# Kernel optimization log

Hardware: AMD Instinct MI355X
Metric: run time of the kernel (lower is better)

The kernel has to match this reference:

```python
import jax, jax.numpy as jnp
import numpy as np

B, T, D, K = 16, 4096, 512, 128
ALPHA_MIN = 1e-06
OMEGA_MAX = float(np.pi)
SN_EPS = 1e-06


def setup_inputs() -> dict:
    key = jax.random.key(0)
    ks = jax.random.split(key, 7)
    x = jax.random.normal(ks[0], (B, T, D), jnp.float32)
    # irregular positive step sizes, mean ~ 1/T like the uniform-grid default
    dt = jax.random.uniform(ks[1], (B, T), jnp.float32, minval=0.1, maxval=1.9) * (1.0 / T)
    # replicate reset_parameters: target_alpha ~ U(0.01, 0.2), raw = log(expm1(alpha - alpha_min))
    target_alpha = jax.random.uniform(ks[2], (K,), jnp.float32, minval=0.01, maxval=0.2)
    s_real_raw = jnp.log(jnp.expm1(jnp.maximum(target_alpha - ALPHA_MIN, 1e-08)))
    s_imag = jax.random.uniform(ks[3], (K,), jnp.float32, minval=-np.pi, maxval=np.pi)
    # kaiming-uniform-ish proj weight [K, D] and bias [K]
    W = jax.random.normal(ks[4], (K, D), jnp.float32) * (1.0 / np.sqrt(D))
    bound = 1.0 / np.sqrt(D)
    bias = jax.random.uniform(ks[5], (K,), jnp.float32, minval=-bound, maxval=bound)
    b_log = jnp.zeros((K,), jnp.float32)  # torch stores [1,1,K]; broadcasting is identical
    u_sn = jax.random.normal(ks[6], (K,), jnp.float32)  # spectral-norm power-iteration vector
    return {"x": x, "dt": dt, "s_real_raw": s_real_raw, "s_imag": s_imag,
            "W": W, "bias": bias, "b_log": b_log, "u_sn": u_sn}


def _spectral_normalize(W, u):
    # one power iteration, u/v detached (as torch.nn.utils.spectral_norm does)
    v = W.T @ u
    v = v / (jnp.linalg.norm(v) + SN_EPS)
    u2 = W @ v
    u2 = u2 / (jnp.linalg.norm(u2) + SN_EPS)
    u2 = jax.lax.stop_gradient(u2)
    v = jax.lax.stop_gradient(v)
    sigma = u2 @ (W @ v)
    return W / sigma


def reference(x, dt, s_real_raw, s_imag, W, bias, b_log, u_sn):
    # x: [B,T,D], dt: [B,T] -> lap_feats [B,T,2K]
    alpha = jax.nn.softplus(s_real_raw) + ALPHA_MIN          # [K] strictly positive decay
    omega = jnp.clip(s_imag, -OMEGA_MAX, OMEGA_MAX)          # [K]
    Wsn = _spectral_normalize(W, u_sn)
    u = jnp.einsum('btd,kd->btk', x, Wsn) + bias             # spectral-norm projection
    dt3 = dt[..., None]                                      # [B,T,1]
    rho = jnp.exp(-alpha * dt3)                              # [B,T,K]
    theta = omega * dt3
    cos_t, sin_t = jnp.cos(theta), jnp.sin(theta)
    b_gain = jnp.exp(b_log)                                  # [K]
    inj = (1.0 - rho) * (b_gain * u)                         # [B,T,K]

    def step(carry, inp):
        c, s = carry
        r, ct, st, it = inp
        c_new = r * (c * ct - s * st) + it
        s_new = r * (c * st + s * ct) + it
        return (c_new, s_new), (c_new, s_new)

    seq = (jnp.moveaxis(rho, 1, 0), jnp.moveaxis(cos_t, 1, 0),
           jnp.moveaxis(sin_t, 1, 0), jnp.moveaxis(inj, 1, 0))  # each [T,B,K]
    init = (jnp.zeros((x.shape[0], K), x.dtype), jnp.zeros((x.shape[0], K), x.dtype))
    _, (C, S) = jax.lax.scan(step, init, seq)
    C = jnp.moveaxis(C, 0, 1)  # [B,T,K]
    S = jnp.moveaxis(S, 0, 1)
    return jnp.concatenate([C, S], axis=-1)
```

## Files before the change

kernel.cpp:

```cpp
#include <hip/hip_runtime.h>
#include <stdint.h>

#define BB 16
#define TT 4096
#define DDIM 512
#define KK 128
#define TCB 128
#define NCB (TT / TCB)
#define PI_F 3.14159265358979323846f

typedef unsigned short u16;
typedef __attribute__((ext_vector_type(8))) short short8;
typedef __attribute__((ext_vector_type(4))) float f32x4;

__device__ __forceinline__ uint32_t cvt_bf16_rn(float f) {
  uint32_t u = __float_as_uint(f);
  return (u + 0x7FFFu + ((u >> 16) & 1u)) >> 16;
}
__device__ __forceinline__ uint32_t pack2(float a, float b) {
  return cvt_bf16_rn(a) | (cvt_bf16_rn(b) << 16);
}
__device__ __forceinline__ uint4 pack8(const float4 f0, const float4 f1) {
  uint4 r;
  r.x = pack2(f0.x, f0.y);
  r.y = pack2(f0.z, f0.w);
  r.z = pack2(f1.x, f1.y);
  r.w = pack2(f1.z, f1.w);
  return r;
}
__device__ __forceinline__ float bf16_to_f32(u16 v) {
  return __uint_as_float(((uint32_t)v) << 16);
}
__device__ __forceinline__ void gload_lds16(const void* g, void* l) {
  __builtin_amdgcn_global_load_lds(
      (const __attribute__((address_space(1))) void*)g,
      (__attribute__((address_space(3))) void*)l, 16, 0, 0);
}

__global__ __launch_bounds__(256) void k_prep(
    const float* __restrict__ W, const float* __restrict__ u_sn,
    const float* __restrict__ s_real_raw, const float* __restrict__ s_imag,
    const float* __restrict__ bias, const float* __restrict__ b_log,
    const float* __restrict__ dt,
    float* __restrict__ params, u16* __restrict__ Wp, float* __restrict__ ct) {
  int gb = blockIdx.x;
  int tid = threadIdx.x;
  if (gb < 64) {
    int idx = gb * 256 + tid;
    int k = idx >> 7;
    int d = (idx & 127) * 4;
    float4 v = *(const float4*)&W[(size_t)k * DDIM + d];
    int tile = d >> 6, dl = d & 63;
    int slot = (dl >> 3) ^ (k & 7);
    int e = dl & 7;
    size_t base = (size_t)tile * 8192 + k * 64 + slot * 8 + e;
    uint2 p;
    p.x = pack2(v.x, v.y);
    p.y = pack2(v.z, v.w);
    *(uint2*)&Wp[base] = p;
  } else if (gb < 80) {
    __shared__ float sc[256];
    int b = gb - 64;
    const float* row = dt + (size_t)b * TT;
    float* orow = ct + (size_t)b * TT;
    float loc[16];
    float s = 0.f;
    int base = tid * 16;
    for (int i = 0; i < 16; ++i) { s += row[base + i]; loc[i] = s; }
    sc[tid] = s;
    __syncthreads();
    for (int off = 1; off < 256; off <<= 1) {
      float v = (tid >= off) ? sc[tid - off] : 0.f;
      __syncthreads();
      sc[tid] += v;
      __syncthreads();
    }
    float excl = sc[tid] - s;
    for (int i = 0; i < 16; ++i) orow[base + i] = excl + loc[i];
  } else {
    __shared__ float su[KK];
    __shared__ float sv[DDIM];
    __shared__ float red[4];
    __shared__ float s_sig;
    if (tid < KK) su[tid] = u_sn[tid];
    __syncthreads();
    for (int rep = 0; rep < 2; ++rep) {
      int d = tid + rep * 256;
      float acc = 0.f;
      for (int k = 0; k < KK; ++k) acc += W[k * DDIM + d] * su[k];
      sv[d] = acc;
    }
    __syncthreads();
    float nn = 0.f;
    for (int rep = 0; rep < 2; ++rep) { float v = sv[tid + rep * 256]; nn += v * v; }
    for (int off = 32; off > 0; off >>= 1) nn += __shfl_down(nn, off, 64);
    if ((tid & 63) == 0) red[tid >> 6] = nn;
    __syncthreads();
    float vn2 = red[0] + red[1] + red[2] + red[3];
    __syncthreads();
    float vinv = 1.f / (sqrtf(vn2) + 1e-6f);
    for (int rep = 0; rep < 2; ++rep) sv[tid + rep * 256] *= vinv;
    __syncthreads();
    float wv = 0.f;
    if (tid < KK) {
      const float* wrow = W + (size_t)tid * DDIM;
      for (int d = 0; d < DDIM; ++d) wv += wrow[d] * sv[d];
    }
    float q = wv * wv;
    for (int off = 32; off > 0; off >>= 1) q += __shfl_down(q, off, 64);
    if ((tid & 63) == 0) red[tid >> 6] = q;
    __syncthreads();
    if (tid == 0) {
      float wn2 = red[0] + red[1] + red[2] + red[3];
      s_sig = wn2 / (sqrtf(wn2) + 1e-6f);
    }
    __syncthreads();
    if (tid < KK) {
      float inv_sigma = 1.f / s_sig;
      float sr = s_real_raw[tid];
      float alpha = ((sr > 20.f) ? sr : log1pf(expf(sr))) + 1e-6f;
      float om = fminf(fmaxf(s_imag[tid], -PI_F), PI_F);
      float bg = expf(b_log[tid]);
      params[tid] = alpha;
      params[KK + tid] = om;
      params[2 * KK + tid] = bg * inv_sigma;
      params[3 * KK + tid] = bg * bias[tid];
    }
  }
}

__global__ __launch_bounds__(512, 4) void k_gemm(
    const float* __restrict__ x, const u16* __restrict__ Wp,
    const float* __restrict__ dt, const float* __restrict__ ct,
    const float* __restrict__ params, u16* __restrict__ itvb,
    float* __restrict__ csum_re, float* __restrict__ csum_im) {
  __shared__ __align__(16) u16 smem[32768];

  const int chunk = blockIdx.x, b = blockIdx.y;
  const int tid = threadIdx.x;
  const int wv = tid >> 6, l = tid & 63;
  const int lm = l & 15, lg = l >> 4;
  const int kw = wv & 1, tw = wv >> 1;
  const int t0 = chunk * TCB;

  const int xr = tid >> 2, xq = (tid & 3) * 16;
  const size_t xbase = ((size_t)b * TT + t0 + xr) * DDIM + xq;
  const int xs0 = ((xq >> 3) ^ (xr & 7)) * 8;
  const int xs1 = (((xq >> 3) + 1) ^ (xr & 7)) * 8;

  f32x4 acc[2][4];
#pragma unroll
  for (int m = 0; m < 2; ++m)
#pragma unroll
    for (int n = 0; n < 4; ++n) acc[m][n] = (f32x4)(0.0f);

  {
    const char* wsg = (const char*)Wp + (size_t)tid * 16;
    char* wd = (char*)smem + 32768 + tid * 16;
    gload_lds16(wsg, wd);
    gload_lds16(wsg + 8192, wd + 8192);
    const float* xp = x + xbase;
    float4 f0 = *(const float4*)(xp + 0);
    float4 f1 = *(const float4*)(xp + 4);
    float4 f2 = *(const float4*)(xp + 8);
    float4 f3 = *(const float4*)(xp + 12);
    *(uint4*)&smem[xr * 64 + xs0] = pack8(f0, f1);
    *(uint4*)&smem[xr * 64 + xs1] = pack8(f2, f3);
  }
  __syncthreads();

  int cur = 0;
  for (int it = 0; it < 8; ++it) {
    float4 f0, f1, f2, f3;
    if (it < 7) {
      const float* xp = x + xbase + (it + 1) * 64;
      f0 = *(const float4*)(xp + 0);
      f1 = *(const float4*)(xp + 4);
      f2 = *(const float4*)(xp + 8);
      f3 = *(const float4*)(xp + 12);
      const char* wsg = (const char*)Wp + (size_t)(it + 1) * 16384 + tid * 16;
      char* wd = (char*)smem + 32768 + (cur ^ 1) * 16384 + tid * 16;
      gload_lds16(wsg, wd);
      gload_lds16(wsg + 8192, wd + 8192);
    }
    __builtin_amdgcn_sched_barrier(0);
    {
      const u16* xb = smem + cur * 8192;
      const u16* wb = smem + 16384 + cur * 8192;
#pragma unroll
      for (int ks = 0; ks < 2; ++ks) {
        short8 fa[2], fb[4];
#pragma unroll
        for (int m = 0; m < 2; ++m) {
          int row = tw * 32 + m * 16 + lm;
          int sw = ((ks * 4 + lg) ^ (row & 7)) * 8;
          fa[m] = *(const short8*)&xb[row * 64 + sw];
        }
#pragma unroll
        for (int n = 0; n < 4; ++n) {
          int row = kw * 64 + n * 16 + lm;
          int sw = ((ks * 4 + lg) ^ (row & 7)) * 8;
          fb[n] = *(const short8*)&wb[row * 64 + sw];
        }
#pragma unroll
        for (int m = 0; m < 2; ++m)
#pragma unroll
          for (int n = 0; n < 4; ++n)
            acc[m][n] = __builtin_amdgcn_mfma_f32_16x16x32_bf16(fa[m], fb[n], acc[m][n], 0, 0, 0);
      }
    }
    __builtin_amdgcn_sched_barrier(0);
    if (it < 7) {
      u16* xb = smem + (cur ^ 1) * 8192;
      *(uint4*)&xb[xr * 64 + xs0] = pack8(f0, f1);
      *(uint4*)&xb[xr * 64 + xs1] = pack8(f2, f3);
    }
    __syncthreads();
    cur ^= 1;
  }

  float* totr = (float*)smem;
  float* toti = (float*)smem + 512;
  u16* litv = smem + 8192;

  float dtv[2][4], ctv[2][4];
#pragma unroll
  for (int m = 0; m < 2; ++m)
#pragma unroll
    for (int r = 0; r < 4; ++r) {
      int t = t0 + tw * 32 + m * 16 + lg * 4 + r;
      dtv[m][r] = dt[(size_t)b * TT + t];
      ctv[m][r] = ct[(size_t)b * TT + t];
    }

#pragma unroll
  for (int n = 0; n < 4; ++n) {
    int k = kw * 64 + n * 16 + lm;
    float pal = params[k], pom = params[KK + k];
    float pc1 = params[2 * KK + k], pc2 = params[3 * KK + k];
    float sr = 0.f, si2 = 0.f;
#pragma unroll
    for (int m = 0; m < 2; ++m)
#pragma unroll
      for (int r = 0; r < 4; ++r) {
        float g = acc[m][n][r];
        float a = pal * dtv[m][r];
        float omr = a * (1.f - a * (0.5f - a * (1.f / 6.f)));
        float itv = omr * (pc1 * g + pc2);
        int tl = tw * 32 + m * 16 + lg * 4 + r;
        litv[tl * KK + k] = (u16)cvt_bf16_rn(itv);
        float e = __expf(pal * ctv[m][r]);
        float sn, cs;
        __sincosf(pom * ctv[m][r], &sn, &cs);
        sr += itv * e * cs;
        si2 -= itv * e * sn;
      }
    sr += __shfl_xor(sr, 16, 64);
    sr += __shfl_xor(sr, 32, 64);
    si2 += __shfl_xor(si2, 16, 64);
    si2 += __shfl_xor(si2, 32, 64);
    if (lg == 0) { totr[tw * KK + k] = sr; toti[tw * KK + k] = si2; }
  }
  __syncthreads();

  if (tid < 256) {
    int v = tid & 127;
    float* src = (tid < 128) ? totr : toti;
    float* dst = (tid < 128) ? csum_re : csum_im;
    dst[((size_t)b * NCB + chunk) * KK + v] =
        (src[v] + src[KK + v]) + (src[2 * KK + v] + src[3 * KK + v]);
  }
  {
    int row = tid >> 4;
    int c8 = (tid & 15) * 8;
#pragma unroll
    for (int rr = 0; rr < 4; ++rr) {
      int tr = rr * 32 + row;
      uint4 v = *(const uint4*)&litv[tr * KK + c8];
      *(uint4*)&itvb[((size_t)b * TT + t0 + tr) * KK + c8] = v;
    }
  }
}

__global__ __launch_bounds__(512) void k_final(
    const u16* __restrict__ itvb, const float* __restrict__ ct,
    const float* __restrict__ params,
    const float* __restrict__ csum_re, const float* __restrict__ csum_im,
    float* __restrict__ out) {
  __shared__ float prer[KK], prei[KK];
  __shared__ float segr[4][KK], segi[4][KK];
  const int chunk = blockIdx.x, b = blockIdx.y;
  const int tid = threadIdx.x;
  const int k = tid & 127, tseg = tid >> 7;
  const int tbase = chunk * TCB + tseg * 32;

  if (tid < 256) {
    int v = tid & 127;
    const float* srcp = (tid < 128) ? csum_re : csum_im;
    float* dstp = (tid < 128) ? prer : prei;
    size_t base = (size_t)b * NCB * KK + v;
    float a0 = 0.f, a1 = 0.f, a2 = 0.f, a3 = 0.f;
    int c = 0;
    for (; c + 4 <= chunk; c += 4) {
      a0 += srcp[base + (size_t)(c + 0) * KK];
      a1 += srcp[base + (size_t)(c + 1) * KK];
      a2 += srcp[base + (size_t)(c + 2) * KK];
      a3 += srcp[base + (size_t)(c + 3) * KK];
    }
    for (; c < chunk; ++c) a0 += srcp[base + (size_t)c * KK];
    dstp[v] = (a0 + a1) + (a2 + a3);
  }

  const float pal = params[k], pom = params[KK + k];
  float sr = 0.f, si = 0.f;
#pragma unroll 4
  for (int i = 0; i < 32; ++i) {
    int t = tbase + i;
    float itv = bf16_to_f32(itvb[((size_t)b * TT + t) * KK + k]);
    float ctv = ct[(size_t)b * TT + t];
    float e = __expf(pal * ctv);
    float sn, cs;
    __sincosf(pom * ctv, &sn, &cs);
    sr += itv * e * cs;
    si -= itv * e * sn;
  }
  segr[tseg][k] = sr;
  segi[tseg][k] = si;
  __syncthreads();
  float cr = prer[k], ci = prei[k];
  for (int s = 0; s < tseg; ++s) { cr += segr[s][k]; ci += segi[s][k]; }
#pragma unroll 4
  for (int i = 0; i < 32; ++i) {
    int t = tbase + i;
    float itv = bf16_to_f32(itvb[((size_t)b * TT + t) * KK + k]);
    float ctv = ct[(size_t)b * TT + t];
    float e = __expf(pal * ctv);
    float sn, cs;
    __sincosf(pom * ctv, &sn, &cs);
    cr += itv * e * cs;
    ci -= itv * e * sn;
    float dec = __builtin_amdgcn_rcpf(e);
    float Rw = dec * (cs * cr - sn * ci);
    float Iw = dec * (cs * ci + sn * cr);
    size_t rowb = ((size_t)b * TT + t) * (2 * KK);
    out[rowb + k] = Rw - Iw;
    out[rowb + KK + k] = Rw + Iw;
  }
}

extern "C" void kernel_launch(void* const* d_in, const int* in_sizes, int n_in,
                              void* d_out, int out_size, void* d_ws, size_t ws_size,
                              hipStream_t stream) {
  const float* x    = (const float*)d_in[0];
  const float* dt   = (const float*)d_in[1];
  const float* srr  = (const float*)d_in[2];
  const float* si   = (const float*)d_in[3];
  const float* W    = (const float*)d_in[4];
  const float* bias = (const float*)d_in[5];
  const float* blog = (const float*)d_in[6];
  const float* usn  = (const float*)d_in[7];
  float* out = (float*)d_out;
  float* ws = (float*)d_ws;

  float* params  = ws;
  float* ct      = ws + 4 * KK;
  float* csum_re = ct + (size_t)BB * TT;
  float* csum_im = csum_re + (size_t)BB * NCB * KK;
  u16*   Wp      = (u16*)(csum_im + (size_t)BB * NCB * KK);
  u16*   itvb    = Wp + 65536;

  k_prep<<<81, 256, 0, stream>>>(W, usn, srr, si, bias, blog, dt, params, Wp, ct);
  k_gemm<<<dim3(NCB, BB), 512, 0, stream>>>(x, Wp, dt, ct, params, itvb,
                                            csum_re, csum_im);
  k_final<<<dim3(NCB, BB), 512, 0, stream>>>(itvb, ct, params,
                                             csum_re, csum_im, out);
}
```

Before: 69.58 us.

## Deepen GEMM x-prefetch pipeline and vectorize final scan over four channels per thread

The projection kernel now prefetches x two K-steps ahead into alternating register sets. Its full __syncthreads is replaced by explicit vmcnt/lgkmcnt waits plus s_barrier, so global loads stay in flight across the MFMA phase. The final kernel gives each thread four adjacent channels and an 8-step time segment (16 segments instead of 4). It uses 8-byte bf16 loads and float4 output stores in place of scalar accesses. This cuts per-element memory instructions and shortens the serial per-thread loop, at the cost of more register pressure and a longer serial prefix sum over segments.

```diff
diff --git a/kernel.cpp b/kernel.cpp
--- a/kernel.cpp
+++ b/kernel.cpp
@@ -27,9 +27,6 @@
   r.z = pack2(f1.x, f1.y);
   r.w = pack2(f1.z, f1.w);
   return r;
-}
-__device__ __forceinline__ float bf16_to_f32(u16 v) {
-  return __uint_as_float(((uint32_t)v) << 16);
 }
 __device__ __forceinline__ void gload_lds16(const void* g, void* l) {
   __builtin_amdgcn_global_load_lds(
@@ -154,39 +151,63 @@
 #pragma unroll
     for (int n = 0; n < 4; ++n) acc[m][n] = (f32x4)(0.0f);
 
+  float4 xa[4], xb[4];
+  const char* wsrc = (const char*)Wp + (size_t)tid * 16;
+  char* wd0 = (char*)smem + 32768 + tid * 16;
+  char* wd1 = wd0 + 16384;
+
   {
-    const char* wsg = (const char*)Wp + (size_t)tid * 16;
-    char* wd = (char*)smem + 32768 + tid * 16;
-    gload_lds16(wsg, wd);
-    gload_lds16(wsg + 8192, wd + 8192);
+    gload_lds16(wsrc, wd0);
+    gload_lds16(wsrc + 8192, wd0 + 8192);
     const float* xp = x + xbase;
-    float4 f0 = *(const float4*)(xp + 0);
-    float4 f1 = *(const float4*)(xp + 4);
-    float4 f2 = *(const float4*)(xp + 8);
-    float4 f3 = *(const float4*)(xp + 12);
-    *(uint4*)&smem[xr * 64 + xs0] = pack8(f0, f1);
-    *(uint4*)&smem[xr * 64 + xs1] = pack8(f2, f3);
-  }
-  __syncthreads();
-
-  int cur = 0;
-  for (int it = 0; it < 8; ++it) {
-    float4 f0, f1, f2, f3;
-    if (it < 7) {
-      const float* xp = x + xbase + (it + 1) * 64;
-      f0 = *(const float4*)(xp + 0);
-      f1 = *(const float4*)(xp + 4);
-      f2 = *(const float4*)(xp + 8);
-      f3 = *(const float4*)(xp + 12);
-      const char* wsg = (const char*)Wp + (size_t)(it + 1) * 16384 + tid * 16;
-      char* wd = (char*)smem + 32768 + (cur ^ 1) * 16384 + tid * 16;
+    xa[0] = *(const float4*)(xp + 0);
+    xa[1] = *(const float4*)(xp + 4);
+    xa[2] = *(const float4*)(xp + 8);
+    xa[3] = *(const float4*)(xp + 12);
+    gload_lds16(wsrc + 16384, wd1);
+    gload_lds16(wsrc + 16384 + 8192, wd1 + 8192);
+    const float* xp1 = x + xbase + 64;
+    xb[0] = *(const float4*)(xp1 + 0);
+    xb[1] = *(const float4*)(xp1 + 4);
+    xb[2] = *(const float4*)(xp1 + 8);
+    xb[3] = *(const float4*)(xp1 + 12);
+    __builtin_amdgcn_sched_barrier(0);
+    asm volatile("s_waitcnt vmcnt(6)" ::: "memory");
+    __builtin_amdgcn_sched_barrier(0);
+    *(uint4*)&smem[xr * 64 + xs0] = pack8(xa[0], xa[1]);
+    *(uint4*)&smem[xr * 64 + xs1] = pack8(xa[2], xa[3]);
+    asm volatile("s_waitcnt lgkmcnt(0)" ::: "memory");
+    __builtin_amdgcn_s_barrier();
+    __builtin_amdgcn_sched_barrier(0);
+  }
+
+#pragma unroll
+  for (int j = 0; j < 8; ++j) {
+    const int p = j & 1;
+    if (j >= 1 && j <= 6) {
+      const char* wsg = (const char*)Wp + (size_t)(j + 1) * 16384 + tid * 16;
+      char* wd = (char*)smem + 32768 + ((j + 1) & 1) * 16384 + tid * 16;
       gload_lds16(wsg, wd);
       gload_lds16(wsg + 8192, wd + 8192);
     }
+    if (j <= 5) {
+      const float* xp = x + xbase + (size_t)(j + 2) * 64;
+      if (p == 0) {
+        xa[0] = *(const float4*)(xp + 0);
+        xa[1] = *(const float4*)(xp + 4);
+        xa[2] = *(const float4*)(xp + 8);
+        xa[3] = *(const float4*)(xp + 12);
+      } else {
+        xb[0] = *(const float4*)(xp + 0);
+        xb[1] = *(const float4*)(xp + 4);
+        xb[2] = *(const float4*)(xp + 8);
+        xb[3] = *(const float4*)(xp + 12);
+      }
+    }
     __builtin_amdgcn_sched_barrier(0);
     {
-      const u16* xb = smem + cur * 8192;
-      const u16* wb = smem + 16384 + cur * 8192;
+      const u16* xbuf = smem + p * 8192;
+      const u16* wbuf = smem + 16384 + p * 8192;
 #pragma unroll
       for (int ks = 0; ks < 2; ++ks) {
         short8 fa[2], fb[4];
@@ -194,13 +215,13 @@
         for (int m = 0; m < 2; ++m) {
           int row = tw * 32 + m * 16 + lm;
           int sw = ((ks * 4 + lg) ^ (row & 7)) * 8;
-          fa[m] = *(const short8*)&xb[row * 64 + sw];
+          fa[m] = *(const short8*)&xbuf[row * 64 + sw];
         }
 #pragma unroll
         for (int n = 0; n < 4; ++n) {
           int row = kw * 64 + n * 16 + lm;
           int sw = ((ks * 4 + lg) ^ (row & 7)) * 8;
-          fb[n] = *(const short8*)&wb[row * 64 + sw];
+          fb[n] = *(const short8*)&wbuf[row * 64 + sw];
         }
 #pragma unroll
         for (int m = 0; m < 2; ++m)
@@ -210,14 +231,24 @@
       }
     }
     __builtin_amdgcn_sched_barrier(0);
-    if (it < 7) {
-      u16* xb = smem + (cur ^ 1) * 8192;
-      *(uint4*)&xb[xr * 64 + xs0] = pack8(f0, f1);
-      *(uint4*)&xb[xr * 64 + xs1] = pack8(f2, f3);
-    }
-    __syncthreads();
-    cur ^= 1;
-  }
+    if (j <= 6) {
+      if (j == 6) asm volatile("s_waitcnt vmcnt(0)" ::: "memory");
+      else        asm volatile("s_waitcnt vmcnt(4)" ::: "memory");
+      __builtin_amdgcn_sched_barrier(0);
+      u16* xw = smem + (p ^ 1) * 8192;
+      if (((j + 1) & 1) == 0) {
+        *(uint4*)&xw[xr * 64 + xs0] = pack8(xa[0], xa[1]);
+        *(uint4*)&xw[xr * 64 + xs1] = pack8(xa[2], xa[3]);
+      } else {
+        *(uint4*)&xw[xr * 64 + xs0] = pack8(xb[0], xb[1]);
+        *(uint4*)&xw[xr * 64 + xs1] = pack8(xb[2], xb[3]);
+      }
+      asm volatile("s_waitcnt lgkmcnt(0)" ::: "memory");
+      __builtin_amdgcn_s_barrier();
+      __builtin_amdgcn_sched_barrier(0);
+    }
+  }
+  __syncthreads();
 
   float* totr = (float*)smem;
   float* toti = (float*)smem + 512;
@@ -288,11 +319,11 @@
     const float* __restrict__ csum_re, const float* __restrict__ csum_im,
     float* __restrict__ out) {
   __shared__ float prer[KK], prei[KK];
-  __shared__ float segr[4][KK], segi[4][KK];
+  __shared__ float segr[16][KK], segi[16][KK];
   const int chunk = blockIdx.x, b = blockIdx.y;
   const int tid = threadIdx.x;
-  const int k = tid & 127, tseg = tid >> 7;
-  const int tbase = chunk * TCB + tseg * 32;
+  const int k4 = (tid & 31) * 4, tseg = tid >> 5;
+  const int tbase = chunk * TCB + tseg * 8;
 
   if (tid < 256) {
     int v = tid & 127;
@@ -311,40 +342,68 @@
     dstp[v] = (a0 + a1) + (a2 + a3);
   }
 
-  const float pal = params[k], pom = params[KK + k];
-  float sr = 0.f, si = 0.f;
-#pragma unroll 4
-  for (int i = 0; i < 32; ++i) {
+  float4 pal4 = *(const float4*)&params[k4];
+  float4 pom4 = *(const float4*)&params[KK + k4];
+  float pal[4] = {pal4.x, pal4.y, pal4.z, pal4.w};
+  float pom[4] = {pom4.x, pom4.y, pom4.z, pom4.w};
+
+  float sr[4] = {0.f, 0.f, 0.f, 0.f}, si[4] = {0.f, 0.f, 0.f, 0.f};
+#pragma unroll
+  for (int i = 0; i < 8; ++i) {
     int t = tbase + i;
-    float itv = bf16_to_f32(itvb[((size_t)b * TT + t) * KK + k]);
     float ctv = ct[(size_t)b * TT + t];
-    float e = __expf(pal * ctv);
-    float sn, cs;
-    __sincosf(pom * ctv, &sn, &cs);
-    sr += itv * e * cs;
-    si -= itv * e * sn;
-  }
-  segr[tseg][k] = sr;
-  segi[tseg][k] = si;
+    uint2 iv = *(const uint2*)&itvb[((size_t)b * TT + t) * KK + k4];
+    float it[4] = {__uint_as_float(iv.x << 16), __uint_as_float(iv.x & 0xFFFF0000u),
+                   __uint_as_float(iv.y << 16), __uint_as_float(iv.y & 0xFFFF0000u)};
+#pragma unroll
+    for (int c = 0; c < 4; ++c) {
+      float e = __expf(pal[c] * ctv);
+      float sn, cs;
+      __sincosf(pom[c] * ctv, &sn, &cs);
+      sr[c] += it[c] * e * cs;
+      si[c] -= it[c] * e * sn;
+    }
+  }
+  *(float4*)&segr[tseg][k4] = make_float4(sr[0], sr[1], sr[2], sr[3]);
+  *(float4*)&segi[tseg][k4] = make_float4(si[0], si[1], si[2], si[3]);
   __syncthreads();
-  float cr = prer[k], ci = prei[k];
-  for (int s = 0; s < tseg; ++s) { cr += segr[s][k]; ci += segi[s][k]; }
-#pragma unroll 4
-  for (int i = 0; i < 32; ++i) {
+  float cr[4], ci[4];
+  {
+    float4 p0 = *(const float4*)&prer[k4];
+    float4 p1 = *(const float4*)&prei[k4];
+    cr[0] = p0.x; cr[1] = p0.y; cr[2] = p0.z; cr[3] = p0.w;
+    ci[0] = p1.x; ci[1] = p1.y; ci[2] = p1.z; ci[3] = p1.w;
+  }
+  for (int s = 0; s < tseg; ++s) {
+    float4 a = *(const float4*)&segr[s][k4];
+    float4 bb = *(const float4*)&segi[s][k4];
+    cr[0] += a.x; cr[1] += a.y; cr[2] += a.z; cr[3] += a.w;
+    ci[0] += bb.x; ci[1] += bb.y; ci[2] += bb.z; ci[3] += bb.w;
+  }
+#pragma unroll
+  for (int i = 0; i < 8; ++i) {
     int t = tbase + i;
-    float itv = bf16_to_f32(itvb[((size_t)b * TT + t) * KK + k]);
     float ctv = ct[(size_t)b * TT + t];
-    float e = __expf(pal * ctv);
-    float sn, cs;
-    __sincosf(pom * ctv, &sn, &cs);
-    cr += itv * e * cs;
-    ci -= itv * e * sn;
-    float dec = __builtin_amdgcn_rcpf(e);
-    float Rw = dec * (cs * cr - sn * ci);
-    float Iw = dec * (cs * ci + sn * cr);
+    uint2 iv = *(const uint2*)&itvb[((size_t)b * TT + t) * KK + k4];
+    float it[4] = {__uint_as_float(iv.x << 16), __uint_as_float(iv.x & 0xFFFF0000u),
+                   __uint_as_float(iv.y << 16), __uint_as_float(iv.y & 0xFFFF0000u)};
+    float C4[4], S4[4];
+#pragma unroll
+    for (int c = 0; c < 4; ++c) {
+      float e = __expf(pal[c] * ctv);
+      float sn, cs;
+      __sincosf(pom[c] * ctv, &sn, &cs);
+      cr[c] += it[c] * e * cs;
+      ci[c] -= it[c] * e * sn;
+      float dec = __builtin_amdgcn_rcpf(e);
+      float Rw = dec * (cs * cr[c] - sn * ci[c]);
+      float Iw = dec * (cs * ci[c] + sn * cr[c]);
+      C4[c] = Rw - Iw;
+      S4[c] = Rw + Iw;
+    }
     size_t rowb = ((size_t)b * TT + t) * (2 * KK);
-    out[rowb + k] = Rw - Iw;
-    out[rowb + KK + k] = Rw + Iw;
+    *(float4*)&out[rowb + k4] = make_float4(C4[0], C4[1], C4[2], C4[3]);
+    *(float4*)&out[rowb + KK + k4] = make_float4(S4[0], S4[1], S4[2], S4[3]);
   }
 }
 
```

Result: slower. 71.18 us (+2.3%).

## Vectorize final scan pass over 4 channels and cache twiddles in registers

Applied to the files above, without the earlier changes.

The final kernel now gives each thread 4 adjacent channels over 8 timesteps instead of 1 channel over 32, with 16 segments per chunk. Loads of the bf16 input and stores of the output become vectorized. The exp/sincos factors and the input values are kept in registers from the first pass, so the second pass does not recompute transcendentals or reload data, and it gets the decay inverse from the squared magnitude of the cached factor. The prep kernel also splits the W·v matvec across all 256 threads, which adds register pressure and a longer serial prefix over 16 segments.

```diff
diff --git a/kernel.cpp b/kernel.cpp
--- a/kernel.cpp
+++ b/kernel.cpp
@@ -27,9 +27,6 @@
   r.z = pack2(f1.x, f1.y);
   r.w = pack2(f1.z, f1.w);
   return r;
-}
-__device__ __forceinline__ float bf16_to_f32(u16 v) {
-  return __uint_as_float(((uint32_t)v) << 16);
 }
 __device__ __forceinline__ void gload_lds16(const void* g, void* l) {
   __builtin_amdgcn_global_load_lds(
@@ -81,6 +78,7 @@
     __shared__ float su[KK];
     __shared__ float sv[DDIM];
     __shared__ float red[4];
+    __shared__ float wred[256];
     __shared__ float s_sig;
     if (tid < KK) su[tid] = u_sn[tid];
     __syncthreads();
@@ -101,11 +99,16 @@
     float vinv = 1.f / (sqrtf(vn2) + 1e-6f);
     for (int rep = 0; rep < 2; ++rep) sv[tid + rep * 256] *= vinv;
     __syncthreads();
+    {
+      int k = tid & 127, q = tid >> 7;
+      const float* wrow = W + (size_t)k * DDIM + q * 256;
+      float p = 0.f;
+      for (int d = 0; d < 256; ++d) p += wrow[d] * sv[q * 256 + d];
+      wred[tid] = p;
+    }
+    __syncthreads();
     float wv = 0.f;
-    if (tid < KK) {
-      const float* wrow = W + (size_t)tid * DDIM;
-      for (int d = 0; d < DDIM; ++d) wv += wrow[d] * sv[d];
-    }
+    if (tid < KK) wv = wred[tid] + wred[tid + 128];
     float q = wv * wv;
     for (int off = 32; off > 0; off >>= 1) q += __shfl_down(q, off, 64);
     if ((tid & 63) == 0) red[tid >> 6] = q;
@@ -288,11 +291,11 @@
     const float* __restrict__ csum_re, const float* __restrict__ csum_im,
     float* __restrict__ out) {
   __shared__ float prer[KK], prei[KK];
-  __shared__ float segr[4][KK], segi[4][KK];
+  __shared__ float segr[16][KK], segi[16][KK];
   const int chunk = blockIdx.x, b = blockIdx.y;
   const int tid = threadIdx.x;
-  const int k = tid & 127, tseg = tid >> 7;
-  const int tbase = chunk * TCB + tseg * 32;
+  const int k4 = (tid & 31) * 4, tseg = tid >> 5;
+  const int tbase = chunk * TCB + tseg * 8;
 
   if (tid < 256) {
     int v = tid & 127;
@@ -311,40 +314,68 @@
     dstp[v] = (a0 + a1) + (a2 + a3);
   }
 
-  const float pal = params[k], pom = params[KK + k];
-  float sr = 0.f, si = 0.f;
-#pragma unroll 4
-  for (int i = 0; i < 32; ++i) {
+  float4 pal4 = *(const float4*)&params[k4];
+  float4 pom4 = *(const float4*)&params[KK + k4];
+  float pal[4] = {pal4.x, pal4.y, pal4.z, pal4.w};
+  float pom[4] = {pom4.x, pom4.y, pom4.z, pom4.w};
+
+  uint2 iv8[8];
+  float fr[8][4], fi[8][4];
+  float sr[4] = {0.f, 0.f, 0.f, 0.f}, si[4] = {0.f, 0.f, 0.f, 0.f};
+#pragma unroll
+  for (int i = 0; i < 8; ++i) {
     int t = tbase + i;
-    float itv = bf16_to_f32(itvb[((size_t)b * TT + t) * KK + k]);
     float ctv = ct[(size_t)b * TT + t];
-    float e = __expf(pal * ctv);
-    float sn, cs;
-    __sincosf(pom * ctv, &sn, &cs);
-    sr += itv * e * cs;
-    si -= itv * e * sn;
-  }
-  segr[tseg][k] = sr;
-  segi[tseg][k] = si;
+    iv8[i] = *(const uint2*)&itvb[((size_t)b * TT + t) * KK + k4];
+    float it[4] = {__uint_as_float(iv8[i].x << 16), __uint_as_float(iv8[i].x & 0xFFFF0000u),
+                   __uint_as_float(iv8[i].y << 16), __uint_as_float(iv8[i].y & 0xFFFF0000u)};
+#pragma unroll
+    for (int c = 0; c < 4; ++c) {
+      float e = __expf(pal[c] * ctv);
+      float sn, cs;
+      __sincosf(pom[c] * ctv, &sn, &cs);
+      fr[i][c] = e * cs;
+      fi[i][c] = e * sn;
+      sr[c] += it[c] * fr[i][c];
+      si[c] -= it[c] * fi[i][c];
+    }
+  }
+  *(float4*)&segr[tseg][k4] = make_float4(sr[0], sr[1], sr[2], sr[3]);
+  *(float4*)&segi[tseg][k4] = make_float4(si[0], si[1], si[2], si[3]);
   __syncthreads();
-  float cr = prer[k], ci = prei[k];
-  for (int s = 0; s < tseg; ++s) { cr += segr[s][k]; ci += segi[s][k]; }
-#pragma unroll 4
-  for (int i = 0; i < 32; ++i) {
+  float cr[4], ci[4];
+  {
+    float4 p0 = *(const float4*)&prer[k4];
+    float4 p1 = *(const float4*)&prei[k4];
+    cr[0] = p0.x; cr[1] = p0.y; cr[2] = p0.z; cr[3] = p0.w;
+    ci[0] = p1.x; ci[1] = p1.y; ci[2] = p1.z; ci[3] = p1.w;
+  }
+  for (int s = 0; s < tseg; ++s) {
+    float4 a = *(const float4*)&segr[s][k4];
+    float4 bb = *(const float4*)&segi[s][k4];
+    cr[0] += a.x; cr[1] += a.y; cr[2] += a.z; cr[3] += a.w;
+    ci[0] += bb.x; ci[1] += bb.y; ci[2] += bb.z; ci[3] += bb.w;
+  }
+#pragma unroll
+  for (int i = 0; i < 8; ++i) {
     int t = tbase + i;
-    float itv = bf16_to_f32(itvb[((size_t)b * TT + t) * KK + k]);
-    float ctv = ct[(size_t)b * TT + t];
-    float e = __expf(pal * ctv);
-    float sn, cs;
-    __sincosf(pom * ctv, &sn, &cs);
-    cr += itv * e * cs;
-    ci -= itv * e * sn;
-    float dec = __builtin_amdgcn_rcpf(e);
-    float Rw = dec * (cs * cr - sn * ci);
-    float Iw = dec * (cs * ci + sn * cr);
+    float it[4] = {__uint_as_float(iv8[i].x << 16), __uint_as_float(iv8[i].x & 0xFFFF0000u),
+                   __uint_as_float(iv8[i].y << 16), __uint_as_float(iv8[i].y & 0xFFFF0000u)};
+    float C4[4], S4[4];
+#pragma unroll
+    for (int c = 0; c < 4; ++c) {
+      float f_r = fr[i][c], f_i = fi[i][c];
+      cr[c] += it[c] * f_r;
+      ci[c] -= it[c] * f_i;
+      float inv = __builtin_amdgcn_rcpf(f_r * f_r + f_i * f_i);
+      float Rw = (cr[c] * f_r - ci[c] * f_i) * inv;
+      float Iw = (cr[c] * f_i + ci[c] * f_r) * inv;
+      C4[c] = Rw - Iw;
+      S4[c] = Rw + Iw;
+    }
     size_t rowb = ((size_t)b * TT + t) * (2 * KK);
-    out[rowb + k] = Rw - Iw;
-    out[rowb + KK + k] = Rw + Iw;
+    *(float4*)&out[rowb + k4] = make_float4(C4[0], C4[1], C4[2], C4[3]);
+    *(float4*)&out[rowb + KK + k4] = make_float4(S4[0], S4[1], S4[2], S4[3]);
   }
 }
 
```

Result: faster. 67.52 us (-3.0%).
